# Kernel tuning notes

Measured on AMD Instinct MI355X. Metric: run time of the kernel, lower is better.

The kernel has to match this reference:

```python
import jax, jax.numpy as jnp
import numpy as np

B, L, D = 2, 2048, 1024
NUM_HEADS = 16
HEAD_DIM = D // NUM_HEADS


def setup_inputs() -> dict:
    key = jax.random.key(0)
    k1, k2 = jax.random.split(key)
    x = jax.random.normal(k1, (B, L, D), dtype=jnp.float32)
    # torch Linear(input_dim, 3*output_dim, bias=False); store as [in, 3*out] for x @ W
    W_qkv = jax.random.normal(k2, (D, 3 * D), dtype=jnp.float32) * (1.0 / np.sqrt(D))
    return {"x": x, "W_qkv": W_qkv}


def reference(x, W_qkv):
    b, l, d = x.shape
    h, hd = NUM_HEADS, HEAD_DIM
    qkv = x @ W_qkv                                  # [B, L, 3*D]
    qkv = qkv.reshape(b, l, 3, h, hd)
    q = jnp.transpose(qkv[:, :, 0], (0, 2, 1, 3))    # [B, H, L, hd]
    k = jnp.transpose(qkv[:, :, 1], (0, 2, 1, 3))
    v = jnp.transpose(qkv[:, :, 2], (0, 2, 1, 3))
    scale = 1.0 / jnp.sqrt(jnp.asarray(hd, dtype=x.dtype))
    scores = jnp.einsum('bhqd,bhkd->bhqk', q, k) * scale   # [B, H, L, L]
    causal = jnp.triu(jnp.ones((l, l), dtype=bool), k=1)   # True above diagonal -> masked
    scores = jnp.where(causal, -jnp.inf, scores)
    attn = jax.nn.softmax(scores, axis=-1)
    # dropout p=0.0 -> identity (eval mode)
    out = jnp.einsum('bhqk,bhkd->bhqd', attn, v)            # [B, H, L, hd]
    out = jnp.transpose(out, (0, 2, 1, 3)).reshape(b, l, h * hd)
    return out
```

## Files before the change

### kernel.cpp

```cpp
#include <hip/hip_runtime.h>
#include <hip/hip_bf16.h>
#include <math.h>

#define NB_L 2048
#define GM 4096
#define GN 3072
#define GK 1024
#define NROWS 65536
#define SCALE_L2E 0.180336880f

typedef float  f4v __attribute__((ext_vector_type(4)));
typedef short  s4v __attribute__((ext_vector_type(4)));
typedef short  s8v __attribute__((ext_vector_type(8)));

#define MFMA_16x16x32(a, b, c) __builtin_amdgcn_mfma_f32_16x16x32_bf16((a), (b), (c), 0, 0, 0)
#define MFMA_16x16x16(a, b, c) __builtin_amdgcn_mfma_f32_16x16x16bf16_1k((a), (b), (c), 0, 0, 0)

static __device__ __forceinline__ unsigned int bfpk(float a, float b) {
    __hip_bfloat162 h = __float22bfloat162_rn(float2{a, b});
    union { __hip_bfloat162 h2; unsigned int u; } cv; cv.h2 = h; return cv.u;
}
static __device__ __forceinline__ unsigned short bf1(float a) {
    union { __hip_bfloat16 h; unsigned short u; } cv; cv.h = __float2bfloat16(a); return cv.u;
}
static __device__ __forceinline__ float bf2f(unsigned short u) {
    union { unsigned int u; float f; } cv; cv.u = ((unsigned int)u) << 16; return cv.f;
}

static __device__ __forceinline__ void gl_lds16(const ushort* g, ushort* l) {
#if defined(__has_builtin) && __has_builtin(__builtin_amdgcn_global_load_lds)
    __builtin_amdgcn_global_load_lds((const __attribute__((address_space(1))) void*)g,
                                     (__attribute__((address_space(3))) void*)l, 16, 0, 0);
#else
    *(s8v*)l = *(const s8v*)g;
#endif
}

__global__ __launch_bounds__(256) void conv_x(const float* __restrict__ X, ushort* __restrict__ Xb) {
    const int i = blockIdx.x * 256 + threadIdx.x;
    const float4 f0 = ((const float4*)X)[2 * i];
    const float4 f1 = ((const float4*)X)[2 * i + 1];
    uint4 u;
    u.x = bfpk(f0.x, f0.y); u.y = bfpk(f0.z, f0.w);
    u.z = bfpk(f1.x, f1.y); u.w = bfpk(f1.z, f1.w);
    ((uint4*)Xb)[i] = u;
}

__global__ __launch_bounds__(256) void conv_wt(const float* __restrict__ W, ushort* __restrict__ Wt) {
    __shared__ __align__(16) ushort T[64][72];
    const int t = threadIdx.x;
    const int k0 = blockIdx.x * 64, n0 = blockIdx.y * 64;
    {
        const int kr = t >> 2, nc0 = (t & 3) * 16;
        const float* src = W + (size_t)(k0 + kr) * GN + n0 + nc0;
#pragma unroll
        for (int u = 0; u < 4; ++u) {
            const float4 v = *(const float4*)(src + 4 * u);
            T[nc0 + 4 * u + 0][kr] = bf1(v.x);
            T[nc0 + 4 * u + 1][kr] = bf1(v.y);
            T[nc0 + 4 * u + 2][kr] = bf1(v.z);
            T[nc0 + 4 * u + 3][kr] = bf1(v.w);
        }
    }
    __syncthreads();
    {
        const int nr = t >> 2, kc0 = (t & 3) * 16;
        ushort* dst = Wt + (size_t)(n0 + nr) * GK + k0 + kc0;
        *(s8v*)dst       = *(const s8v*)&T[nr][kc0];
        *(s8v*)(dst + 8) = *(const s8v*)&T[nr][kc0 + 8];
    }
}

__global__ __launch_bounds__(256) void qkv_gemm_bf16(
    const ushort* __restrict__ Xb, const ushort* __restrict__ Wt, ushort* __restrict__ Qkv)
{
    __shared__ __align__(16) ushort As[2][4][128][8];
    __shared__ __align__(16) ushort Bs[2][4][128][8];
    const int tid = threadIdx.x;
    const int row0 = blockIdx.y * 128, col0 = blockIdx.x * 128;
    const int mA = tid & 127, k2a = tid >> 7;
    const int lane = tid & 63, w = tid >> 6;
    const int wr = w >> 1, wc = w & 1, lq = lane & 15, quad = lane >> 4;

    f4v acc[4][4];
#pragma unroll
    for (int g = 0; g < 4; ++g)
#pragma unroll
        for (int j = 0; j < 4; ++j) acc[g][j] = 0.f;

    const ushort* gA = Xb + (size_t)(row0 + mA) * GK + k2a * 8;
    const ushort* gB = Wt + (size_t)(col0 + mA) * GK + k2a * 8;

    gl_lds16(gA,      &As[0][k2a][mA][0]);
    gl_lds16(gA + 16, &As[0][k2a + 2][mA][0]);
    gl_lds16(gB,      &Bs[0][k2a][mA][0]);
    gl_lds16(gB + 16, &Bs[0][k2a + 2][mA][0]);

    for (int it = 0; it < 32; ++it) {
        const int cur = it & 1, nxt = cur ^ 1;
        __syncthreads();
        if (it + 1 < 32) {
            const int k0 = (it + 1) * 32;
            gl_lds16(gA + k0,      &As[nxt][k2a][mA][0]);
            gl_lds16(gA + k0 + 16, &As[nxt][k2a + 2][mA][0]);
            gl_lds16(gB + k0,      &Bs[nxt][k2a][mA][0]);
            gl_lds16(gB + k0 + 16, &Bs[nxt][k2a + 2][mA][0]);
        }

        s8v af[4], bfr[4];
#pragma unroll
        for (int g = 0; g < 4; ++g) af[g]  = *(const s8v*)&As[cur][quad][wr * 64 + g * 16 + lq][0];
#pragma unroll
        for (int j = 0; j < 4; ++j) bfr[j] = *(const s8v*)&Bs[cur][quad][wc * 64 + j * 16 + lq][0];
#pragma unroll
        for (int g = 0; g < 4; ++g)
#pragma unroll
            for (int j = 0; j < 4; ++j)
                acc[g][j] = MFMA_16x16x32(af[g], bfr[j], acc[g][j]);
    }

    const float qscale = (col0 < 1024) ? SCALE_L2E : 1.0f;
#pragma unroll
    for (int g = 0; g < 4; ++g)
#pragma unroll
        for (int j = 0; j < 4; ++j) {
            const int col = col0 + wc * 64 + j * 16 + lq;
#pragma unroll
            for (int r = 0; r < 4; ++r) {
                const int row = row0 + wr * 64 + g * 16 + quad * 4 + r;
                Qkv[(size_t)row * GN + col] = bf1(acc[g][j][r] * qscale);
            }
        }
}

__global__ __launch_bounds__(256, 4) void attn_bf16(
    const ushort* __restrict__ Qkv, ushort* __restrict__ Opart, float* __restrict__ Lp)
{
    __shared__ __align__(16) ushort Ks[2][8][64][8];
    __shared__ __align__(16) ushort Vt[2][64][72];

    const int x = blockIdx.x;
    const int bh = x & 31;
    const int qlow = (x >> 5) & 7;
    const int s = (x >> 8) & 1;
    const int x9 = (x >> 9) & 1;
    const int qt = x9 ? (15 - qlow) : qlow;
    const int h = bh & 15, b = bh >> 4;

    const int tid = threadIdx.x;
    const int w = tid >> 6, lane = tid & 63;
    const int lq = lane & 15, quad = lane >> 4;
    const int boff = b * NB_L;
    const int qrow_base = qt * 128 + w * 32;
    const int diag = 2 * qt + (w >> 1);

    s8v qf[2][2];
#pragma unroll
    for (int qg = 0; qg < 2; ++qg)
#pragma unroll
        for (int sb = 0; sb < 2; ++sb)
            qf[qg][sb] = *(const s8v*)(Qkv + (size_t)(boff + qrow_base + qg * 16 + lq) * GN
                                       + h * 64 + sb * 32 + quad * 8);

    f4v o[4][2];
#pragma unroll
    for (int dg = 0; dg < 4; ++dg)
#pragma unroll
        for (int qg = 0; qg < 2; ++qg) o[dg][qg] = 0.f;
    float l_s[2] = {0.f, 0.f};

    const int kt_lo = s ? (qt + 1) : 0;
    const int kt_hi = s ? (2 * qt + 1) : qt;
    const int niter = kt_hi - kt_lo + 1;

    const int pr  = tid >> 2;
    const int dc0 = (tid & 3) * 16, dc4 = tid & 3;
    const int vcol = (2 * pr + 16 * dc4) & 63;
    const int t2 = tid & 127;
    const int krow_s = t2 >> 1, g0 = (t2 & 1) * 4;

    auto compute = [&](int ktc, int bufi) {
        if (ktc > diag) return;
        f4v st[4][2];
#pragma unroll
        for (int kg = 0; kg < 4; ++kg)
#pragma unroll
            for (int qg = 0; qg < 2; ++qg) st[kg][qg] = 0.f;
#pragma unroll
        for (int kg = 0; kg < 4; ++kg) {
#pragma unroll
            for (int sb = 0; sb < 2; ++sb) {
                const s8v af = *(const s8v*)&Ks[bufi][sb * 4 + quad][kg * 16 + lq][0];
#pragma unroll
                for (int qg = 0; qg < 2; ++qg)
                    st[kg][qg] = MFMA_16x16x32(af, qf[qg][sb], st[kg][qg]);
            }
        }
        if (ktc == diag) {
#pragma unroll
            for (int kg = 0; kg < 4; ++kg)
#pragma unroll
                for (int qg = 0; qg < 2; ++qg) {
                    const int qrow = qrow_base + qg * 16 + lq;
#pragma unroll
                    for (int r = 0; r < 4; ++r)
                        if (ktc * 64 + kg * 16 + quad * 4 + r > qrow)
                            st[kg][qg][r] = -INFINITY;
                }
        }
#pragma unroll
        for (int qg = 0; qg < 2; ++qg) {
            float sum = 0.f;
#pragma unroll
            for (int kg = 0; kg < 4; ++kg)
#pragma unroll
                for (int r = 0; r < 4; ++r) {
                    const float p = exp2f(st[kg][qg][r]);
                    st[kg][qg][r] = p;
                    sum += p;
                }
            sum += __shfl_xor(sum, 16);
            sum += __shfl_xor(sum, 32);
            l_s[qg] += sum;
        }
#pragma unroll
        for (int ks = 0; ks < 4; ++ks) {
            s4v pb[2];
#pragma unroll
            for (int qg = 0; qg < 2; ++qg) {
                union { s4v v; uint2 u; } c;
                c.u.x = bfpk(st[ks][qg][0], st[ks][qg][1]);
                c.u.y = bfpk(st[ks][qg][2], st[ks][qg][3]);
                pb[qg] = c.v;
            }
#pragma unroll
            for (int dg = 0; dg < 4; ++dg) {
                const s4v va = *(const s4v*)&Vt[bufi][dg * 16 + lq][((ks + dg) & 3) * 16 + quad * 4];
#pragma unroll
                for (int qg = 0; qg < 2; ++qg)
                    o[dg][qg] = MFMA_16x16x16(va, pb[qg], o[dg][qg]);
            }
        }
    };

    s8v preg[4];
    if (tid < 128) {
        const ushort* vp = Qkv + (size_t)(boff + kt_lo * 64 + 2 * pr) * GN + 2048 + h * 64 + dc0;
        preg[0] = *(const s8v*)vp;        preg[1] = *(const s8v*)(vp + 8);
        preg[2] = *(const s8v*)(vp + GN); preg[3] = *(const s8v*)(vp + GN + 8);
    } else {
        const ushort* kp = Qkv + (size_t)(boff + kt_lo * 64 + krow_s) * GN + 1024 + h * 64 + g0 * 8;
#pragma unroll
        for (int i = 0; i < 4; ++i) preg[i] = *(const s8v*)(kp + 8 * i);
    }

    for (int i = 0; i < niter; ++i) {
        const int wb = i & 1;
        __syncthreads();
        if (tid < 128) {
#pragma unroll
            for (int j = 0; j < 16; ++j) {
                const unsigned short lo = (unsigned short)((j < 8) ? preg[0][j] : preg[1][j - 8]);
                const unsigned short hi = (unsigned short)((j < 8) ? preg[2][j] : preg[3][j - 8]);
                *(unsigned int*)&Vt[wb][dc0 + j][vcol] = (unsigned int)lo | ((unsigned int)hi << 16);
            }
        } else {
#pragma unroll
            for (int i2 = 0; i2 < 4; ++i2)
                *(s8v*)&Ks[wb][g0 + i2][krow_s][0] = preg[i2];
        }
        if (i + 1 < niter) {
            const int ktn = kt_lo + i + 1;
            if (tid < 128) {
                const ushort* vp = Qkv + (size_t)(boff + ktn * 64 + 2 * pr) * GN + 2048 + h * 64 + dc0;
                preg[0] = *(const s8v*)vp;        preg[1] = *(const s8v*)(vp + 8);
                preg[2] = *(const s8v*)(vp + GN); preg[3] = *(const s8v*)(vp + GN + 8);
            } else {
                const ushort* kp = Qkv + (size_t)(boff + ktn * 64 + krow_s) * GN + 1024 + h * 64 + g0 * 8;
#pragma unroll
                for (int i2 = 0; i2 < 4; ++i2) preg[i2] = *(const s8v*)(kp + 8 * i2);
            }
        }
        if (i > 0) compute(kt_lo + i - 1, wb ^ 1);
    }
    __syncthreads();
    compute(kt_hi, (niter - 1) & 1);

#pragma unroll
    for (int qg = 0; qg < 2; ++qg) {
        const size_t prow = (size_t)(s * 32 + bh) * 2048 + qrow_base + qg * 16 + lq;
#pragma unroll
        for (int dg = 0; dg < 4; ++dg) {
            const int d = dg * 16 + quad * 4;
            uint2 u;
            u.x = bfpk(o[dg][qg][0], o[dg][qg][1]);
            u.y = bfpk(o[dg][qg][2], o[dg][qg][3]);
            *(uint2*)&Opart[prow * 64 + d] = u;
        }
        if (quad == 0) Lp[prow] = l_s[qg];
    }
}

__global__ __launch_bounds__(256) void attn_combine(
    const ushort* __restrict__ Opart, const float* __restrict__ Lp, float* __restrict__ Out)
{
    const int id = blockIdx.x * 256 + threadIdx.x;
    const int row = id >> 4, c4 = (id & 15) * 4;
    const float l0 = Lp[row], l1 = Lp[row + NROWS];
    const float inv = 1.0f / (l0 + l1);

    const s4v a = *(const s4v*)&Opart[(size_t)row * 64 + c4];
    const s4v c = *(const s4v*)&Opart[(size_t)(row + NROWS) * 64 + c4];
    float4 v;
    v.x = (bf2f((unsigned short)a[0]) + bf2f((unsigned short)c[0])) * inv;
    v.y = (bf2f((unsigned short)a[1]) + bf2f((unsigned short)c[1])) * inv;
    v.z = (bf2f((unsigned short)a[2]) + bf2f((unsigned short)c[2])) * inv;
    v.w = (bf2f((unsigned short)a[3]) + bf2f((unsigned short)c[3])) * inv;

    const int bh = row >> 11, qrow = row & 2047;
    const int b = bh >> 4, h = bh & 15;
    *(float4*)(Out + ((size_t)(b * 2048 + qrow)) * 1024 + h * 64 + c4) = v;
}

extern "C" void kernel_launch(void* const* d_in, const int* in_sizes, int n_in,
                              void* d_out, int out_size, void* d_ws, size_t ws_size,
                              hipStream_t stream)
{
    const float* x  = (const float*)d_in[0];
    const float* wq = (const float*)d_in[1];
    float* out = (float*)d_out;

    ushort* wsp  = (ushort*)d_ws;
    ushort* qkvb = wsp;
    ushort* xb   = wsp + (size_t)GM * GN;
    ushort* wt   = xb + (size_t)GM * GK;
    ushort* opart = wsp + (size_t)GM * GN;
    float*  lp    = (float*)(opart + (size_t)2 * NROWS * 64);

    conv_x<<<GM * GK / (256 * 8), 256, 0, stream>>>(x, xb);
    conv_wt<<<dim3(GK / 64, GN / 64), 256, 0, stream>>>(wq, wt);
    qkv_gemm_bf16<<<dim3(GN / 128, GM / 128), 256, 0, stream>>>(xb, wt, qkvb);
    attn_bf16<<<1024, 256, 0, stream>>>(qkvb, opart, lp);
    attn_combine<<<NROWS * 16 / 256, 256, 0, stream>>>(opart, lp, out);
}
```

Baseline: 200.1 us.

## Write head-major swizzled Q/K/V^T from GEMM and stage K/V via direct LDS loads

The QKV GEMM epilogue now writes Q, K and a transposed V into per-head contiguous buffers, with XOR swizzles on K and V^T. This lets the attention kernel copy K and V tiles straight into LDS with global_load_lds instead of loading into registers and transposing V by hand. The attention kernel also computes the softmax row sums with an MFMA against a ones vector, replacing the shuffle reductions. The cost moves to the GEMM epilogue, whose V^T stores are strided and poorly coalesced.

```diff
diff --git a/kernel.cpp b/kernel.cpp
--- a/kernel.cpp
+++ b/kernel.cpp
@@ -28,12 +28,8 @@
 }
 
 static __device__ __forceinline__ void gl_lds16(const ushort* g, ushort* l) {
-#if defined(__has_builtin) && __has_builtin(__builtin_amdgcn_global_load_lds)
     __builtin_amdgcn_global_load_lds((const __attribute__((address_space(1))) void*)g,
                                      (__attribute__((address_space(3))) void*)l, 16, 0, 0);
-#else
-    *(s8v*)l = *(const s8v*)g;
-#endif
 }
 
 __global__ __launch_bounds__(256) void conv_x(const float* __restrict__ X, ushort* __restrict__ Xb) {
@@ -72,7 +68,8 @@
 }
 
 __global__ __launch_bounds__(256) void qkv_gemm_bf16(
-    const ushort* __restrict__ Xb, const ushort* __restrict__ Wt, ushort* __restrict__ Qkv)
+    const ushort* __restrict__ Xb, const ushort* __restrict__ Wt,
+    ushort* __restrict__ Qh, ushort* __restrict__ Kh, ushort* __restrict__ VT)
 {
     __shared__ __align__(16) ushort As[2][4][128][8];
     __shared__ __align__(16) ushort Bs[2][4][128][8];
@@ -106,7 +103,6 @@
             gl_lds16(gB + k0,      &Bs[nxt][k2a][mA][0]);
             gl_lds16(gB + k0 + 16, &Bs[nxt][k2a + 2][mA][0]);
         }
-
         s8v af[4], bfr[4];
 #pragma unroll
         for (int g = 0; g < 4; ++g) af[g]  = *(const s8v*)&As[cur][quad][wr * 64 + g * 16 + lq][0];
@@ -119,25 +115,35 @@
                 acc[g][j] = MFMA_16x16x32(af[g], bfr[j], acc[g][j]);
     }
 
-    const float qscale = (col0 < 1024) ? SCALE_L2E : 1.0f;
+    const int part = blockIdx.x >> 3;
 #pragma unroll
     for (int g = 0; g < 4; ++g)
 #pragma unroll
         for (int j = 0; j < 4; ++j) {
-            const int col = col0 + wc * 64 + j * 16 + lq;
+            const int col = (col0 & 1023) + wc * 64 + j * 16 + lq;
+            const int hh = col >> 6, d = col & 63;
 #pragma unroll
             for (int r = 0; r < 4; ++r) {
                 const int row = row0 + wr * 64 + g * 16 + quad * 4 + r;
-                Qkv[(size_t)row * GN + col] = bf1(acc[g][j][r] * qscale);
+                const int b = row >> 11, tok = row & 2047;
+                const int bh = b * 16 + hh;
+                if (part == 0) {
+                    Qh[((size_t)bh * 2048 + tok) * 64 + d] = bf1(acc[g][j][r] * SCALE_L2E);
+                } else if (part == 1) {
+                    Kh[((size_t)bh * 2048 + tok) * 64 + (d ^ ((tok & 7) << 3))] = bf1(acc[g][j][r]);
+                } else {
+                    VT[((size_t)bh * 64 + d) * 2048 + (tok ^ ((d & 7) << 3))] = bf1(acc[g][j][r]);
+                }
             }
         }
 }
 
 __global__ __launch_bounds__(256, 4) void attn_bf16(
-    const ushort* __restrict__ Qkv, ushort* __restrict__ Opart, float* __restrict__ Lp)
+    const ushort* __restrict__ Qh, const ushort* __restrict__ Kh,
+    const ushort* __restrict__ VT, ushort* __restrict__ Opart, float* __restrict__ Lp)
 {
-    __shared__ __align__(16) ushort Ks[2][8][64][8];
-    __shared__ __align__(16) ushort Vt[2][64][72];
+    __shared__ __align__(16) ushort Ks[2][64 * 64];
+    __shared__ __align__(16) ushort Vt[2][64 * 64];
 
     const int x = blockIdx.x;
     const int bh = x & 31;
@@ -145,12 +151,11 @@
     const int s = (x >> 8) & 1;
     const int x9 = (x >> 9) & 1;
     const int qt = x9 ? (15 - qlow) : qlow;
-    const int h = bh & 15, b = bh >> 4;
 
     const int tid = threadIdx.x;
     const int w = tid >> 6, lane = tid & 63;
     const int lq = lane & 15, quad = lane >> 4;
-    const int boff = b * NB_L;
+    const int kswz = (lq & 7) << 3;
     const int qrow_base = qt * 128 + w * 32;
     const int diag = 2 * qt + (w >> 1);
 
@@ -159,25 +164,35 @@
     for (int qg = 0; qg < 2; ++qg)
 #pragma unroll
         for (int sb = 0; sb < 2; ++sb)
-            qf[qg][sb] = *(const s8v*)(Qkv + (size_t)(boff + qrow_base + qg * 16 + lq) * GN
-                                       + h * 64 + sb * 32 + quad * 8);
+            qf[qg][sb] = *(const s8v*)(Qh + ((size_t)bh * 2048 + qrow_base + qg * 16 + lq) * 64
+                                       + sb * 32 + quad * 8);
 
     f4v o[4][2];
 #pragma unroll
     for (int dg = 0; dg < 4; ++dg)
 #pragma unroll
         for (int qg = 0; qg < 2; ++qg) o[dg][qg] = 0.f;
-    float l_s[2] = {0.f, 0.f};
+    f4v lacc[2]; lacc[0] = 0.f; lacc[1] = 0.f;
+    const s4v ones = { (short)0x3F80, (short)0x3F80, (short)0x3F80, (short)0x3F80 };
 
     const int kt_lo = s ? (qt + 1) : 0;
     const int kt_hi = s ? (2 * qt + 1) : qt;
     const int niter = kt_hi - kt_lo + 1;
 
-    const int pr  = tid >> 2;
-    const int dc0 = (tid & 3) * 16, dc4 = tid & 3;
-    const int vcol = (2 * pr + 16 * dc4) & 63;
-    const int t2 = tid & 127;
-    const int krow_s = t2 >> 1, g0 = (t2 & 1) * 4;
+    const ushort* kbase = Kh + (size_t)bh * 2048 * 64;
+    const ushort* vbase = VT + (size_t)bh * 64 * 2048;
+    const int g1 = tid, g2 = tid + 256;
+    const int kr1 = g1 >> 3, ko1 = (g1 & 7) * 8;
+    const int kr2 = g2 >> 3, ko2 = (g2 & 7) * 8;
+
+    auto stage = [&](int kt, int bufi) {
+        const ushort* kt_k = kbase + (size_t)kt * 64 * 64;
+        const ushort* kt_v = vbase + kt * 64;
+        gl_lds16(kt_k + kr1 * 64 + ko1,          &Ks[bufi][g1 * 8]);
+        gl_lds16(kt_k + kr2 * 64 + ko2,          &Ks[bufi][g2 * 8]);
+        gl_lds16(kt_v + (size_t)kr1 * 2048 + ko1, &Vt[bufi][g1 * 8]);
+        gl_lds16(kt_v + (size_t)kr2 * 2048 + ko2, &Vt[bufi][g2 * 8]);
+    };
 
     auto compute = [&](int ktc, int bufi) {
         if (ktc > diag) return;
@@ -187,15 +202,15 @@
 #pragma unroll
             for (int qg = 0; qg < 2; ++qg) st[kg][qg] = 0.f;
 #pragma unroll
-        for (int kg = 0; kg < 4; ++kg) {
+        for (int kg = 0; kg < 4; ++kg)
 #pragma unroll
             for (int sb = 0; sb < 2; ++sb) {
-                const s8v af = *(const s8v*)&Ks[bufi][sb * 4 + quad][kg * 16 + lq][0];
+                const s8v af = *(const s8v*)&Ks[bufi][(kg * 16 + lq) * 64
+                                                     + ((sb * 32 + quad * 8) ^ kswz)];
 #pragma unroll
                 for (int qg = 0; qg < 2; ++qg)
                     st[kg][qg] = MFMA_16x16x32(af, qf[qg][sb], st[kg][qg]);
             }
-        }
         if (ktc == diag) {
 #pragma unroll
             for (int kg = 0; kg < 4; ++kg)
@@ -209,20 +224,12 @@
                 }
         }
 #pragma unroll
-        for (int qg = 0; qg < 2; ++qg) {
-            float sum = 0.f;
-#pragma unroll
-            for (int kg = 0; kg < 4; ++kg)
-#pragma unroll
-                for (int r = 0; r < 4; ++r) {
-                    const float p = exp2f(st[kg][qg][r]);
-                    st[kg][qg][r] = p;
-                    sum += p;
-                }
-            sum += __shfl_xor(sum, 16);
-            sum += __shfl_xor(sum, 32);
-            l_s[qg] += sum;
-        }
+        for (int kg = 0; kg < 4; ++kg)
+#pragma unroll
+            for (int qg = 0; qg < 2; ++qg)
+#pragma unroll
+                for (int r = 0; r < 4; ++r)
+                    st[kg][qg][r] = exp2f(st[kg][qg][r]);
 #pragma unroll
         for (int ks = 0; ks < 4; ++ks) {
             s4v pb[2];
@@ -234,8 +241,12 @@
                 pb[qg] = c.v;
             }
 #pragma unroll
+            for (int qg = 0; qg < 2; ++qg)
+                lacc[qg] = MFMA_16x16x16(ones, pb[qg], lacc[qg]);
+#pragma unroll
             for (int dg = 0; dg < 4; ++dg) {
-                const s4v va = *(const s4v*)&Vt[bufi][dg * 16 + lq][((ks + dg) & 3) * 16 + quad * 4];
+                const s4v va = *(const s4v*)&Vt[bufi][(dg * 16 + lq) * 64
+                                                     + ((ks * 16 + quad * 4) ^ kswz)];
 #pragma unroll
                 for (int qg = 0; qg < 2; ++qg)
                     o[dg][qg] = MFMA_16x16x16(va, pb[qg], o[dg][qg]);
@@ -243,48 +254,13 @@
         }
     };
 
-    s8v preg[4];
-    if (tid < 128) {
-        const ushort* vp = Qkv + (size_t)(boff + kt_lo * 64 + 2 * pr) * GN + 2048 + h * 64 + dc0;
-        preg[0] = *(const s8v*)vp;        preg[1] = *(const s8v*)(vp + 8);
-        preg[2] = *(const s8v*)(vp + GN); preg[3] = *(const s8v*)(vp + GN + 8);
-    } else {
-        const ushort* kp = Qkv + (size_t)(boff + kt_lo * 64 + krow_s) * GN + 1024 + h * 64 + g0 * 8;
-#pragma unroll
-        for (int i = 0; i < 4; ++i) preg[i] = *(const s8v*)(kp + 8 * i);
-    }
-
+    stage(kt_lo, 0);
     for (int i = 0; i < niter; ++i) {
-        const int wb = i & 1;
+        const int cur = i & 1;
         __syncthreads();
-        if (tid < 128) {
-#pragma unroll
-            for (int j = 0; j < 16; ++j) {
-                const unsigned short lo = (unsigned short)((j < 8) ? preg[0][j] : preg[1][j - 8]);
-                const unsigned short hi = (unsigned short)((j < 8) ? preg[2][j] : preg[3][j - 8]);
-                *(unsigned int*)&Vt[wb][dc0 + j][vcol] = (unsigned int)lo | ((unsigned int)hi << 16);
-            }
-        } else {
-#pragma unroll
-            for (int i2 = 0; i2 < 4; ++i2)
-                *(s8v*)&Ks[wb][g0 + i2][krow_s][0] = preg[i2];
-        }
-        if (i + 1 < niter) {
-            const int ktn = kt_lo + i + 1;
-            if (tid < 128) {
-                const ushort* vp = Qkv + (size_t)(boff + ktn * 64 + 2 * pr) * GN + 2048 + h * 64 + dc0;
-                preg[0] = *(const s8v*)vp;        preg[1] = *(const s8v*)(vp + 8);
-                preg[2] = *(const s8v*)(vp + GN); preg[3] = *(const s8v*)(vp + GN + 8);
-            } else {
-                const ushort* kp = Qkv + (size_t)(boff + ktn * 64 + krow_s) * GN + 1024 + h * 64 + g0 * 8;
-#pragma unroll
-                for (int i2 = 0; i2 < 4; ++i2) preg[i2] = *(const s8v*)(kp + 8 * i2);
-            }
-        }
-        if (i > 0) compute(kt_lo + i - 1, wb ^ 1);
-    }
-    __syncthreads();
-    compute(kt_hi, (niter - 1) & 1);
+        if (i + 1 < niter) stage(kt_lo + i + 1, cur ^ 1);
+        compute(kt_lo + i, cur);
+    }
 
 #pragma unroll
     for (int qg = 0; qg < 2; ++qg) {
@@ -297,7 +273,7 @@
             u.y = bfpk(o[dg][qg][2], o[dg][qg][3]);
             *(uint2*)&Opart[prow * 64 + d] = u;
         }
-        if (quad == 0) Lp[prow] = l_s[qg];
+        if (quad == 0) Lp[prow] = lacc[qg][0];
     }
 }
 
@@ -330,16 +306,19 @@
     const float* wq = (const float*)d_in[1];
     float* out = (float*)d_out;
 
-    ushort* wsp  = (ushort*)d_ws;
-    ushort* qkvb = wsp;
-    ushort* xb   = wsp + (size_t)GM * GN;
-    ushort* wt   = xb + (size_t)GM * GK;
-    ushort* opart = wsp + (size_t)GM * GN;
+    const size_t HEADTEN = (size_t)32 * 2048 * 64;
+    ushort* wsp = (ushort*)d_ws;
+    ushort* qh = wsp;
+    ushort* kh = qh + HEADTEN;
+    ushort* vt = kh + HEADTEN;
+    ushort* xb = vt + HEADTEN;
+    ushort* wt = xb + (size_t)GM * GK;
+    ushort* opart = xb;
     float*  lp    = (float*)(opart + (size_t)2 * NROWS * 64);
 
     conv_x<<<GM * GK / (256 * 8), 256, 0, stream>>>(x, xb);
     conv_wt<<<dim3(GK / 64, GN / 64), 256, 0, stream>>>(wq, wt);
-    qkv_gemm_bf16<<<dim3(GN / 128, GM / 128), 256, 0, stream>>>(xb, wt, qkvb);
-    attn_bf16<<<1024, 256, 0, stream>>>(qkvb, opart, lp);
+    qkv_gemm_bf16<<<dim3(GN / 128, GM / 128), 256, 0, stream>>>(xb, wt, qh, kh, vt);
+    attn_bf16<<<1024, 256, 0, stream>>>(qh, kh, vt, opart, lp);
     attn_combine<<<NROWS * 16 / 256, 256, 0, stream>>>(opart, lp, out);
 }
```

Result: faster. 189.6 us (-5.2%).
